# Kernel tuning notes

Hardware: AMD Instinct MI355X
Metric: run time of the kernel (lower is better)

## Reference

```python
import jax, jax.numpy as jnp
import numpy as np

N_NODES = 100000
N_EDGES = 1600000
IN_CH = 128
OUT_CH = 64
POS_DIM = 64


def setup_inputs() -> dict:
    key = jax.random.key(0)
    k1, k2, k3, k4, k5, k6, k7 = jax.random.split(key, 7)
    x = jax.random.normal(k1, (N_NODES, IN_CH), dtype=jnp.float32)
    edge_index = jax.random.randint(k2, (2, N_EDGES), 0, N_NODES, dtype=jnp.int32)
    pos_encoding = jax.random.normal(k3, (N_NODES, POS_DIM), dtype=jnp.float32)
    # GCNConv linear weight + bias (PyG stores weight [in, out] applied as x @ W)
    W = jax.random.normal(k4, (IN_CH, OUT_CH), dtype=jnp.float32) / np.sqrt(IN_CH)
    b = jax.random.normal(k5, (OUT_CH,), dtype=jnp.float32) * 0.01
    # positional encoding Linear(pos_dim, out_channels)
    Wp = jax.random.normal(k6, (POS_DIM, OUT_CH), dtype=jnp.float32) / np.sqrt(POS_DIM)
    bp = jax.random.normal(k7, (OUT_CH,), dtype=jnp.float32) * 0.01
    return {"x": x, "edge_index": edge_index, "pos_encoding": pos_encoding,
            "W": W, "b": b, "Wp": Wp, "bp": bp}


def reference(x, edge_index, pos_encoding, W, b, Wp, bp):
    N = x.shape[0]
    # --- GCNConv: add self-loops, symmetric normalization ---
    loops = jnp.arange(N, dtype=edge_index.dtype)
    src = jnp.concatenate([edge_index[0], loops])  # [E+N]
    dst = jnp.concatenate([edge_index[1], loops])  # [E+N]
    ones = jnp.ones(src.shape[0], dtype=x.dtype)
    deg = jax.ops.segment_sum(ones, dst, num_segments=N)  # in-degree of A+I
    deg_inv_sqrt = jnp.where(deg > 0, jax.lax.rsqrt(deg), 0.0)
    norm = deg_inv_sqrt[src] * deg_inv_sqrt[dst]  # [E+N]
    # transform first (in->out), then gather/normalize/scatter in out dim
    h = x @ W  # [N, out]
    msg = h[src] * norm[:, None]  # gather + scale, [E+N, out]
    out = jax.ops.segment_sum(msg, dst, num_segments=N) + b  # scatter-add + bias
    # --- positional encoding add ---
    out = out + (pos_encoding @ Wp + bp)
    return out
```

## Files before the change

### kernel.cpp

```cpp
#include <hip/hip_runtime.h>
#include <hip/hip_fp8.h>


#define THREADS 256
#define K_BUCKETS 512
#define BW 196
#define BSTRIDE 4096
#define CHUNK 4096
#define PADK 136
#define PADW 72

typedef __attribute__((ext_vector_type(8))) short s16x8;
typedef __attribute__((ext_vector_type(4))) float f32x4;

__device__ __forceinline__ unsigned short f2bf(float f) {
    unsigned int u = __float_as_uint(f);
    u = (u + 0x7FFFu + ((u >> 16) & 1u)) >> 16;
    return (unsigned short)u;
}

#if defined(__has_builtin)
#if __has_builtin(__builtin_amdgcn_cvt_f32_fp8) && __has_builtin(__builtin_amdgcn_cvt_pk_fp8_f32)
#define HW_FP8 1
#endif
#endif

template <int SEL>
__device__ __forceinline__ float fp8dec(unsigned int v) {
#ifdef HW_FP8
    return __builtin_amdgcn_cvt_f32_fp8(v, SEL);
#else
    __hip_fp8_e4m3 q;
    q.__x = (__hip_fp8_storage_t)((v >> (SEL * 8)) & 0xffu);
    return (float)q;
#endif
}

__device__ __forceinline__ unsigned int fp8enc4(float f0, float f1, float f2, float f3) {
#ifdef HW_FP8
    int p = __builtin_amdgcn_cvt_pk_fp8_f32(f0, f1, 0, false);
    p = __builtin_amdgcn_cvt_pk_fp8_f32(f2, f3, p, true);
    return (unsigned int)p;
#else
    __hip_fp8_e4m3 a(f0), b(f1), c(f2), d(f3);
    return (unsigned int)a.__x | ((unsigned int)b.__x << 8) |
           ((unsigned int)c.__x << 16) | ((unsigned int)d.__x << 24);
#endif
}

__global__ void __launch_bounds__(256)
binscatter_kernel(const int* __restrict__ src, const int* __restrict__ dst,
                  int* __restrict__ cursor, int* __restrict__ binned, int E) {
    __shared__ int hist[K_BUCKETS];
    __shared__ int basew[K_BUCKETS];
    int t = threadIdx.x;
    for (int i = t; i < K_BUCKETS; i += 256) hist[i] = 0;
    __syncthreads();
    int e0 = blockIdx.x * CHUNK;
    for (int i = t; i < CHUNK; i += 256) {
        int e = e0 + i;
        if (e < E) atomicAdd(&hist[dst[e] / BW], 1);
    }
    __syncthreads();
    for (int i = t; i < K_BUCKETS; i += 256) {
        int c = hist[i];
        basew[i] = i * BSTRIDE + (c ? atomicAdd(&cursor[i], c) : 0);
    }
    __syncthreads();
    for (int i = t; i < K_BUCKETS; i += 256) hist[i] = 0;
    __syncthreads();
    for (int i = t; i < CHUNK; i += 256) {
        int e = e0 + i;
        if (e < E) {
            int d = dst[e];
            int k = d / BW;
            int r = atomicAdd(&hist[k], 1);
            binned[basew[k] + r] = src[e] | ((d - k * BW) << 17);
        }
    }
}

__global__ void __launch_bounds__(256)
bucket_csr_kernel(const int* __restrict__ binned, const int* __restrict__ cursor,
                  int* __restrict__ csr_src, int* __restrict__ cnt,
                  int* __restrict__ offs, float* __restrict__ dinv, int N) {
    __shared__ int cnt_l[256];
    __shared__ int scan_l[256];
    __shared__ int cur_l[256];
    __shared__ int csr_l[BSTRIDE];
    int b = blockIdx.x, t = threadIdx.x;
    int nb = cursor[b];
    int base = b * BSTRIDE;
    int node0 = b * BW;
    cnt_l[t] = 0;
    cur_l[t] = 0;
    __syncthreads();
    for (int i = t; i < nb; i += 256) {
        int e = binned[base + i];
        atomicAdd(&cnt_l[e >> 17], 1);
    }
    __syncthreads();
    scan_l[t] = cnt_l[t];
    __syncthreads();
    for (int off = 1; off < 256; off <<= 1) {
        int v = (t >= off) ? scan_l[t - off] : 0;
        __syncthreads();
        scan_l[t] += v;
        __syncthreads();
    }
    for (int i = t; i < nb; i += 256) {
        int e = binned[base + i];
        int ld = e >> 17;
        int pos = (ld ? scan_l[ld - 1] : 0) + atomicAdd(&cur_l[ld], 1);
        csr_l[pos] = e & 0x1FFFF;
    }
    __syncthreads();
    for (int i = t; i < nb; i += 256) csr_src[base + i] = csr_l[i];
    if (t < BW) {
        int node = node0 + t;
        if (node < N) {
            int c = cnt_l[t];
            cnt[node] = c;
            offs[node] = base + (t ? scan_l[t - 1] : 0);
            dinv[node] = rsqrtf((float)(c + 1));
        }
    }
}

__global__ void __launch_bounds__(256)
gemmout_kernel(const float* __restrict__ x, const float* __restrict__ W,
               const float* __restrict__ pos, const float* __restrict__ Wp,
               const float* __restrict__ b, const float* __restrict__ bp,
               const float* __restrict__ dinv, unsigned char* __restrict__ h8,
               float* __restrict__ out, int N) {
    __shared__ unsigned short ldsWT[64 * PADK];
    __shared__ unsigned short ldsWpT[64 * PADW];
    __shared__ float bb[64];
    int t = threadIdx.x;
    for (int i = t; i < 128 * 64; i += 256) {
        int k = i >> 6, n = i & 63;
        ldsWT[n * PADK + k] = f2bf(W[i]);
    }
    for (int i = t; i < 64 * 64; i += 256) {
        int k = i >> 6, c = i & 63;
        ldsWpT[c * PADW + k] = f2bf(Wp[i]);
    }
    if (t < 64) bb[t] = b[t] + bp[t];
    __syncthreads();

    int wave = t >> 6;
    int lane = t & 63;
    int lm = lane & 15;
    int kg = lane >> 4;
    int m = blockIdx.x * 64 + wave * 16 + lm;
    int mload = (m < N) ? m : N - 1;
    const float* xrow = x + (size_t)mload * 128;
    const float* prow = pos + (size_t)mload * 64;

    f32x4 accH0 = {0.f, 0.f, 0.f, 0.f};
    f32x4 accH1 = accH0, accH2 = accH0, accH3 = accH0;
#pragma unroll
    for (int ks = 0; ks < 4; ++ks) {
        int k0 = ks * 32 + kg * 8;
        float4 xa = *(const float4*)(xrow + k0);
        float4 xb = *(const float4*)(xrow + k0 + 4);
        s16x8 bfrag;
        bfrag[0] = (short)f2bf(xa.x); bfrag[1] = (short)f2bf(xa.y);
        bfrag[2] = (short)f2bf(xa.z); bfrag[3] = (short)f2bf(xa.w);
        bfrag[4] = (short)f2bf(xb.x); bfrag[5] = (short)f2bf(xb.y);
        bfrag[6] = (short)f2bf(xb.z); bfrag[7] = (short)f2bf(xb.w);
        s16x8 a0 = *(const s16x8*)&ldsWT[(0  + lm) * PADK + k0];
        s16x8 a1 = *(const s16x8*)&ldsWT[(16 + lm) * PADK + k0];
        s16x8 a2 = *(const s16x8*)&ldsWT[(32 + lm) * PADK + k0];
        s16x8 a3 = *(const s16x8*)&ldsWT[(48 + lm) * PADK + k0];
        accH0 = __builtin_amdgcn_mfma_f32_16x16x32_bf16(a0, bfrag, accH0, 0, 0, 0);
        accH1 = __builtin_amdgcn_mfma_f32_16x16x32_bf16(a1, bfrag, accH1, 0, 0, 0);
        accH2 = __builtin_amdgcn_mfma_f32_16x16x32_bf16(a2, bfrag, accH2, 0, 0, 0);
        accH3 = __builtin_amdgcn_mfma_f32_16x16x32_bf16(a3, bfrag, accH3, 0, 0, 0);
    }

    f32x4 accP0 = {0.f, 0.f, 0.f, 0.f};
    f32x4 accP1 = accP0, accP2 = accP0, accP3 = accP0;
#pragma unroll
    for (int ks = 0; ks < 2; ++ks) {
        int k0 = ks * 32 + kg * 8;
        float4 xa = *(const float4*)(prow + k0);
        float4 xb = *(const float4*)(prow + k0 + 4);
        s16x8 bfrag;
        bfrag[0] = (short)f2bf(xa.x); bfrag[1] = (short)f2bf(xa.y);
        bfrag[2] = (short)f2bf(xa.z); bfrag[3] = (short)f2bf(xa.w);
        bfrag[4] = (short)f2bf(xb.x); bfrag[5] = (short)f2bf(xb.y);
        bfrag[6] = (short)f2bf(xb.z); bfrag[7] = (short)f2bf(xb.w);
        s16x8 a0 = *(const s16x8*)&ldsWpT[(0  + lm) * PADW + k0];
        s16x8 a1 = *(const s16x8*)&ldsWpT[(16 + lm) * PADW + k0];
        s16x8 a2 = *(const s16x8*)&ldsWpT[(32 + lm) * PADW + k0];
        s16x8 a3 = *(const s16x8*)&ldsWpT[(48 + lm) * PADW + k0];
        accP0 = __builtin_amdgcn_mfma_f32_16x16x32_bf16(a0, bfrag, accP0, 0, 0, 0);
        accP1 = __builtin_amdgcn_mfma_f32_16x16x32_bf16(a1, bfrag, accP1, 0, 0, 0);
        accP2 = __builtin_amdgcn_mfma_f32_16x16x32_bf16(a2, bfrag, accP2, 0, 0, 0);
        accP3 = __builtin_amdgcn_mfma_f32_16x16x32_bf16(a3, bfrag, accP3, 0, 0, 0);
    }

    if (m < N) {
        float di = dinv[m];
        float dd = di * di;
        unsigned char* hr = h8 + (size_t)m * 64 + kg * 4;
        float* orow = out + (size_t)m * 64 + kg * 4;
        f32x4 o;
        *(unsigned int*)(hr + 0) =
            fp8enc4(accH0[0] * di, accH0[1] * di, accH0[2] * di, accH0[3] * di);
        o[0] = accP0[0] + bb[kg * 4 + 0] + dd * accH0[0];
        o[1] = accP0[1] + bb[kg * 4 + 1] + dd * accH0[1];
        o[2] = accP0[2] + bb[kg * 4 + 2] + dd * accH0[2];
        o[3] = accP0[3] + bb[kg * 4 + 3] + dd * accH0[3];
        *(f32x4*)(orow + 0) = o;
        *(unsigned int*)(hr + 16) =
            fp8enc4(accH1[0] * di, accH1[1] * di, accH1[2] * di, accH1[3] * di);
        o[0] = accP1[0] + bb[16 + kg * 4 + 0] + dd * accH1[0];
        o[1] = accP1[1] + bb[16 + kg * 4 + 1] + dd * accH1[1];
        o[2] = accP1[2] + bb[16 + kg * 4 + 2] + dd * accH1[2];
        o[3] = accP1[3] + bb[16 + kg * 4 + 3] + dd * accH1[3];
        *(f32x4*)(orow + 16) = o;
        *(unsigned int*)(hr + 32) =
            fp8enc4(accH2[0] * di, accH2[1] * di, accH2[2] * di, accH2[3] * di);
        o[0] = accP2[0] + bb[32 + kg * 4 + 0] + dd * accH2[0];
        o[1] = accP2[1] + bb[32 + kg * 4 + 1] + dd * accH2[1];
        o[2] = accP2[2] + bb[32 + kg * 4 + 2] + dd * accH2[2];
        o[3] = accP2[3] + bb[32 + kg * 4 + 3] + dd * accH2[3];
        *(f32x4*)(orow + 32) = o;
        *(unsigned int*)(hr + 48) =
            fp8enc4(accH3[0] * di, accH3[1] * di, accH3[2] * di, accH3[3] * di);
        o[0] = accP3[0] + bb[48 + kg * 4 + 0] + dd * accH3[0];
        o[1] = accP3[1] + bb[48 + kg * 4 + 1] + dd * accH3[1];
        o[2] = accP3[2] + bb[48 + kg * 4 + 2] + dd * accH3[2];
        o[3] = accP3[3] + bb[48 + kg * 4 + 3] + dd * accH3[3];
        *(f32x4*)(orow + 48) = o;
    }
}

__global__ void __launch_bounds__(256)
gather_kernel(const int* __restrict__ csr_src, const int* __restrict__ offs,
              const int* __restrict__ cnt, const unsigned char* __restrict__ h8,
              const float* __restrict__ dinv, float* __restrict__ out, int N) {
    int wid = (int)((blockIdx.x * (size_t)blockDim.x + threadIdx.x) >> 6);
    int lane = threadIdx.x & 63;
    if (wid >= N) return;
    int g = lane >> 4;
    int cl = lane & 15;
    int beg = offs[wid];
    int num = cnt[wid];
    const int* idx = csr_src + beg;
    const unsigned char* hbase = h8 + cl * 4;
    float a0 = 0.f, a1 = 0.f, a2 = 0.f, a3 = 0.f;
    float b0 = 0.f, b1 = 0.f, b2 = 0.f, b3 = 0.f;
    int j = 0;
    for (; j + 16 <= num; j += 16) {
        int s0 = idx[j + g];
        int s1 = idx[j + 4 + g];
        int s2 = idx[j + 8 + g];
        int s3 = idx[j + 12 + g];
        unsigned int v0 = *(const unsigned int*)(hbase + (size_t)s0 * 64);
        unsigned int v1 = *(const unsigned int*)(hbase + (size_t)s1 * 64);
        unsigned int v2 = *(const unsigned int*)(hbase + (size_t)s2 * 64);
        unsigned int v3 = *(const unsigned int*)(hbase + (size_t)s3 * 64);
        a0 += fp8dec<0>(v0); a1 += fp8dec<1>(v0); a2 += fp8dec<2>(v0); a3 += fp8dec<3>(v0);
        b0 += fp8dec<0>(v1); b1 += fp8dec<1>(v1); b2 += fp8dec<2>(v1); b3 += fp8dec<3>(v1);
        a0 += fp8dec<0>(v2); a1 += fp8dec<1>(v2); a2 += fp8dec<2>(v2); a3 += fp8dec<3>(v2);
        b0 += fp8dec<0>(v3); b1 += fp8dec<1>(v3); b2 += fp8dec<2>(v3); b3 += fp8dec<3>(v3);
    }
    for (; j + 4 <= num; j += 4) {
        int s = idx[j + g];
        unsigned int v = *(const unsigned int*)(hbase + (size_t)s * 64);
        a0 += fp8dec<0>(v); a1 += fp8dec<1>(v); a2 += fp8dec<2>(v); a3 += fp8dec<3>(v);
    }
    int rem = num - j;
    if (g < rem) {
        int s = idx[j + g];
        unsigned int v = *(const unsigned int*)(hbase + (size_t)s * 64);
        a0 += fp8dec<0>(v); a1 += fp8dec<1>(v); a2 += fp8dec<2>(v); a3 += fp8dec<3>(v);
    }
    a0 += b0; a1 += b1; a2 += b2; a3 += b3;
    a0 += __shfl_xor(a0, 32); a1 += __shfl_xor(a1, 32);
    a2 += __shfl_xor(a2, 32); a3 += __shfl_xor(a3, 32);
    a0 += __shfl_xor(a0, 16); a1 += __shfl_xor(a1, 16);
    a2 += __shfl_xor(a2, 16); a3 += __shfl_xor(a3, 16);
    if (g == 0) {
        float di = dinv[wid];
        float* orow = out + (size_t)wid * 64 + cl * 4;
        float4 o = *(const float4*)orow;
        o.x = fmaf(di, a0, o.x);
        o.y = fmaf(di, a1, o.y);
        o.z = fmaf(di, a2, o.z);
        o.w = fmaf(di, a3, o.w);
        *(float4*)orow = o;
    }
}

extern "C" void kernel_launch(void* const* d_in, const int* in_sizes, int n_in,
                              void* d_out, int out_size, void* d_ws, size_t ws_size,
                              hipStream_t stream) {
    const float* x   = (const float*)d_in[0];
    const int*   ei  = (const int*)d_in[1];
    const float* pos = (const float*)d_in[2];
    const float* W   = (const float*)d_in[3];
    const float* b   = (const float*)d_in[4];
    const float* Wp  = (const float*)d_in[5];
    const float* bp  = (const float*)d_in[6];
    float* out = (float*)d_out;

    const int N = in_sizes[0] / 128;
    const int E = in_sizes[1] / 2;
    const int* srcp = ei;
    const int* dstp = ei + E;

    unsigned char* h8    = (unsigned char*)d_ws;
    float* dinv          = (float*)d_ws + (size_t)N * 32;
    int*   cnt           = (int*)(dinv + N);
    int*   offs          = cnt + N;
    int*   cursor        = offs + N;
    int*   csr_src       = cursor + K_BUCKETS;
    int*   binned        = (int*)d_ws;

    (void)hipMemsetAsync(cursor, 0, K_BUCKETS * sizeof(int), stream);

    int nbHB = (E + CHUNK - 1) / CHUNK;
    binscatter_kernel<<<nbHB, THREADS, 0, stream>>>(srcp, dstp, cursor, binned, E);
    bucket_csr_kernel<<<K_BUCKETS, THREADS, 0, stream>>>(binned, cursor,
                                                         csr_src, cnt, offs, dinv, N);

    int nbGm = (N + 63) / 64;
    gemmout_kernel<<<nbGm, THREADS, 0, stream>>>(x, W, pos, Wp, b, bp, dinv,
                                                 h8, out, N);

    long long totalGC = (long long)N * 64;
    int nbGa = (int)((totalGC + THREADS - 1) / THREADS);
    gather_kernel<<<nbGa, THREADS, 0, stream>>>(csr_src, offs, cnt, h8, dinv, out, N);
}
```

Baseline: 119.1 us.

## Pad per-node CSR segments to 16 with zero-row sentinel and pack offset/count

Each node's neighbor list in the bucketed CSR is padded up to a multiple of 16. The padding slots hold a sentinel index N, which points to an extra all-zero row appended to the fp8 feature table. That lets the gather kernel drop its 4-wide and remainder tail loops and run one uniform 16-wide loop. The per-node offset and padded iteration count are packed into a single 32-bit word, replacing the separate cnt and offs arrays and saving one load per node. In exchange, the bucket stride doubles, the kernel does extra gathers of the (cache-resident) zero row, and the shared CSR buffer must be initialized to the sentinel.

```diff
diff --git a/kernel.cpp b/kernel.cpp
--- a/kernel.cpp
+++ b/kernel.cpp
@@ -5,7 +5,7 @@
 #define THREADS 256
 #define K_BUCKETS 512
 #define BW 196
-#define BSTRIDE 4096
+#define BSTRIDE 8192
 #define CHUNK 4096
 #define PADK 136
 #define PADW 72
@@ -82,8 +82,8 @@
 
 __global__ void __launch_bounds__(256)
 bucket_csr_kernel(const int* __restrict__ binned, const int* __restrict__ cursor,
-                  int* __restrict__ csr_src, int* __restrict__ cnt,
-                  int* __restrict__ offs, float* __restrict__ dinv, int N) {
+                  int* __restrict__ csr_src, int* __restrict__ offsw,
+                  float* __restrict__ dinv, int N) {
     __shared__ int cnt_l[256];
     __shared__ int scan_l[256];
     __shared__ int cur_l[256];
@@ -94,13 +94,15 @@
     int node0 = b * BW;
     cnt_l[t] = 0;
     cur_l[t] = 0;
+    for (int i = t; i < BSTRIDE; i += 256) csr_l[i] = N;
     __syncthreads();
     for (int i = t; i < nb; i += 256) {
         int e = binned[base + i];
         atomicAdd(&cnt_l[e >> 17], 1);
     }
     __syncthreads();
-    scan_l[t] = cnt_l[t];
+    int creal = cnt_l[t];
+    scan_l[t] = (creal + 15) & ~15;
     __syncthreads();
     for (int off = 1; off < 256; off <<= 1) {
         int v = (t >= off) ? scan_l[t - off] : 0;
@@ -115,14 +117,15 @@
         csr_l[pos] = e & 0x1FFFF;
     }
     __syncthreads();
-    for (int i = t; i < nb; i += 256) csr_src[base + i] = csr_l[i];
+    int tot = scan_l[255];
+    for (int i = t; i < tot; i += 256) csr_src[base + i] = csr_l[i];
     if (t < BW) {
         int node = node0 + t;
         if (node < N) {
-            int c = cnt_l[t];
-            cnt[node] = c;
-            offs[node] = base + (t ? scan_l[t - 1] : 0);
-            dinv[node] = rsqrtf((float)(c + 1));
+            int pstart = t ? scan_l[t - 1] : 0;
+            int pc = ((creal + 15) & ~15) >> 4;
+            offsw[node] = (base + pstart) | (pc << 24);
+            dinv[node] = rsqrtf((float)(creal + 1));
         }
     }
 }
@@ -137,6 +140,8 @@
     __shared__ unsigned short ldsWpT[64 * PADW];
     __shared__ float bb[64];
     int t = threadIdx.x;
+    if (blockIdx.x == 0 && t < 16)
+        ((unsigned int*)(h8 + (size_t)N * 64))[t] = 0;
     for (int i = t; i < 128 * 64; i += 256) {
         int k = i >> 6, n = i & 63;
         ldsWT[n * PADK + k] = f2bf(W[i]);
@@ -239,26 +244,27 @@
 }
 
 __global__ void __launch_bounds__(256)
-gather_kernel(const int* __restrict__ csr_src, const int* __restrict__ offs,
-              const int* __restrict__ cnt, const unsigned char* __restrict__ h8,
-              const float* __restrict__ dinv, float* __restrict__ out, int N) {
+gather_kernel(const int* __restrict__ csr_src, const int* __restrict__ offsw,
+              const unsigned char* __restrict__ h8, const float* __restrict__ dinv,
+              float* __restrict__ out, int N) {
     int wid = (int)((blockIdx.x * (size_t)blockDim.x + threadIdx.x) >> 6);
     int lane = threadIdx.x & 63;
     if (wid >= N) return;
     int g = lane >> 4;
     int cl = lane & 15;
-    int beg = offs[wid];
-    int num = cnt[wid];
-    const int* idx = csr_src + beg;
+    unsigned int w = (unsigned int)offsw[wid];
+    int beg = (int)(w & 0x00FFFFFFu);
+    int it = (int)(w >> 24);
+    const int* idx = csr_src + beg + g;
     const unsigned char* hbase = h8 + cl * 4;
     float a0 = 0.f, a1 = 0.f, a2 = 0.f, a3 = 0.f;
     float b0 = 0.f, b1 = 0.f, b2 = 0.f, b3 = 0.f;
-    int j = 0;
-    for (; j + 16 <= num; j += 16) {
-        int s0 = idx[j + g];
-        int s1 = idx[j + 4 + g];
-        int s2 = idx[j + 8 + g];
-        int s3 = idx[j + 12 + g];
+    for (int i = 0; i < it; ++i) {
+        int s0 = idx[0];
+        int s1 = idx[4];
+        int s2 = idx[8];
+        int s3 = idx[12];
+        idx += 16;
         unsigned int v0 = *(const unsigned int*)(hbase + (size_t)s0 * 64);
         unsigned int v1 = *(const unsigned int*)(hbase + (size_t)s1 * 64);
         unsigned int v2 = *(const unsigned int*)(hbase + (size_t)s2 * 64);
@@ -267,17 +273,6 @@
         b0 += fp8dec<0>(v1); b1 += fp8dec<1>(v1); b2 += fp8dec<2>(v1); b3 += fp8dec<3>(v1);
         a0 += fp8dec<0>(v2); a1 += fp8dec<1>(v2); a2 += fp8dec<2>(v2); a3 += fp8dec<3>(v2);
         b0 += fp8dec<0>(v3); b1 += fp8dec<1>(v3); b2 += fp8dec<2>(v3); b3 += fp8dec<3>(v3);
-    }
-    for (; j + 4 <= num; j += 4) {
-        int s = idx[j + g];
-        unsigned int v = *(const unsigned int*)(hbase + (size_t)s * 64);
-        a0 += fp8dec<0>(v); a1 += fp8dec<1>(v); a2 += fp8dec<2>(v); a3 += fp8dec<3>(v);
-    }
-    int rem = num - j;
-    if (g < rem) {
-        int s = idx[j + g];
-        unsigned int v = *(const unsigned int*)(hbase + (size_t)s * 64);
-        a0 += fp8dec<0>(v); a1 += fp8dec<1>(v); a2 += fp8dec<2>(v); a3 += fp8dec<3>(v);
     }
     a0 += b0; a1 += b1; a2 += b2; a3 += b3;
     a0 += __shfl_xor(a0, 32); a1 += __shfl_xor(a1, 32);
@@ -314,10 +309,9 @@
     const int* dstp = ei + E;
 
     unsigned char* h8    = (unsigned char*)d_ws;
-    float* dinv          = (float*)d_ws + (size_t)N * 32;
-    int*   cnt           = (int*)(dinv + N);
-    int*   offs          = cnt + N;
-    int*   cursor        = offs + N;
+    float* dinv          = (float*)d_ws + (size_t)(N + 1) * 16;
+    int*   offsw         = (int*)(dinv + N);
+    int*   cursor        = offsw + N;
     int*   csr_src       = cursor + K_BUCKETS;
     int*   binned        = (int*)d_ws;
 
@@ -326,7 +320,7 @@
     int nbHB = (E + CHUNK - 1) / CHUNK;
     binscatter_kernel<<<nbHB, THREADS, 0, stream>>>(srcp, dstp, cursor, binned, E);
     bucket_csr_kernel<<<K_BUCKETS, THREADS, 0, stream>>>(binned, cursor,
-                                                         csr_src, cnt, offs, dinv, N);
+                                                         csr_src, offsw, dinv, N);
 
     int nbGm = (N + 63) / 64;
     gemmout_kernel<<<nbGm, THREADS, 0, stream>>>(x, W, pos, Wp, b, bp, dinv,
@@ -334,5 +328,5 @@
 
     long long totalGC = (long long)N * 64;
     int nbGa = (int)((totalGC + THREADS - 1) / THREADS);
-    gather_kernel<<<nbGa, THREADS, 0, stream>>>(csr_src, offs, cnt, h8, dinv, out, N);
-}
+    gather_kernel<<<nbGa, THREADS, 0, stream>>>(csr_src, offsw, h8, dinv, out, N);
+}
```

Result: faster. 111.5 us (-6.4%).
